# Kernel tuning notes

Measured on AMD Instinct MI355X. Metric: run time of the kernel, lower is better.

The kernel has to match this reference:

```python
import jax, jax.numpy as jnp
import numpy as np

B, N, H = 4, 1024, 32


def setup_inputs() -> dict:
    key = jax.random.key(0)
    ks = jax.random.split(key, 8)
    weights = jax.random.uniform(ks[0], (B, N), dtype=jnp.float32)
    distances = jax.random.uniform(ks[1], (B, N, N), dtype=jnp.float32)
    # nn.Linear-style params (kaiming-uniform-ish scale: U(-1/sqrt(fan_in), 1/sqrt(fan_in)))
    def lin(k, fan_in, fan_out):
        k1, k2 = jax.random.split(k)
        bound = 1.0 / np.sqrt(fan_in)
        W = jax.random.uniform(k1, (fan_in, fan_out), minval=-bound, maxval=bound, dtype=jnp.float32)
        b = jax.random.uniform(k2, (fan_out,), minval=-bound, maxval=bound, dtype=jnp.float32)
        return W, b
    W1, b1 = lin(ks[2], 3, H)
    W2, b2 = lin(ks[3], H, H)
    W3, b3 = lin(ks[4], H, 1)
    return {"weights": weights, "distances": distances,
            "W1": W1, "b1": b1, "W2": W2, "b2": b2, "W3": W3, "b3": b3}


def reference(weights, distances, W1, b1, W2, b2, W3, b3):
    # Avoid materializing the stacked [B,N,N,3] tensor: since the first layer
    # is linear, split W1 rows and broadcast-add the three contributions.
    # h1[b,i,j,:] = w_i * W1[0] + w_j * W1[1] + d_ij * W1[2] + b1
    wi = weights[:, :, None, None] * W1[0]            # [B,N,1,H]
    wj = weights[:, None, :, None] * W1[1]            # [B,1,N,H]
    h = wi + wj + distances[..., None] * W1[2] + b1   # [B,N,N,H]
    h = jax.nn.relu(h)
    h = jax.nn.relu(jnp.einsum('bijh,hk->bijk', h, W2) + b2)
    out = jnp.einsum('bijh,ho->bijo', h, W3) + b3     # [B,N,N,1]
    return jax.nn.softplus(out[..., 0])               # [B,N,N]
```

## Files before the change

kernel.cpp:

```cpp
#include <hip/hip_runtime.h>

#define HCH 32
#define NDIM 1024
#define SEG 512
#define ITERS (SEG / 32)

using half2v  = __attribute__((ext_vector_type(2))) _Float16;
using half8   = __attribute__((ext_vector_type(8))) _Float16;
using floatx4 = __attribute__((ext_vector_type(4))) float;

__global__ __launch_bounds__(256, 4)
void lf_kernel(const float* __restrict__ weights,
               const float* __restrict__ distances,
               const float* __restrict__ W1,
               const float* __restrict__ b1,
               const float* __restrict__ W2,
               const float* __restrict__ b2,
               const float* __restrict__ W3,
               const float* __restrict__ b3,
               float* __restrict__ out)
{
    const int lane = threadIdx.x & 63;
    const int wave_gid = __builtin_amdgcn_readfirstlane(blockIdx.x * 4 + (threadIdx.x >> 6));
    const int row_id = wave_gid >> 1;
    const int j_begin = (wave_gid & 1) * SEG;
    const int b = row_id >> 10;

    const int px = lane & 15;
    const int quad = lane >> 4;
    const int kb = quad * 8;

    const float wi = weights[row_id];

    half2v base2[4], cc2[4], ee2[4];
#pragma unroll
    for (int p = 0; p < 4; ++p) {
        const int chA = kb + 2 * p;
        const int chB = chA + 1;
        base2[p] = half2v{(_Float16)fmaf(W1[chA], wi, b1[chA]),
                          (_Float16)fmaf(W1[chB], wi, b1[chB])};
        cc2[p] = half2v{(_Float16)W1[HCH + chA], (_Float16)W1[HCH + chB]};
        ee2[p] = half2v{(_Float16)W1[2 * HCH + chA], (_Float16)W1[2 * HCH + chB]};
    }

    half8 a_lo, a_hi;
#pragma unroll
    for (int j = 0; j < 8; ++j) {
        a_lo[j] = (_Float16)W2[(kb + j) * HCH + px];
        a_hi[j] = (_Float16)W2[(kb + j) * HCH + 16 + px];
    }

    floatx4 ci_lo, ci_hi;
    float w3lo[4], w3hi[4];
#pragma unroll
    for (int r = 0; r < 4; ++r) {
        ci_lo[r] = b2[quad * 4 + r];
        ci_hi[r] = b2[16 + quad * 4 + r];
        w3lo[r]  = W3[quad * 4 + r];
        w3hi[r]  = W3[16 + quad * 4 + r];
    }
    const float b3v = b3[0];

    const float* __restrict__ drow = distances + (size_t)row_id * NDIM + j_begin;
    const float* __restrict__ wrow = weights + b * NDIM + j_begin;
    float* __restrict__ orow = out + (size_t)row_id * NDIM + j_begin;

    float dbuf[2][2], wbuf[2][2];
#pragma unroll
    for (int t = 0; t < 2; ++t) {
        dbuf[t][0] = drow[t * 32 + px];
        dbuf[t][1] = drow[t * 32 + 16 + px];
        wbuf[t][0] = wrow[t * 32 + px];
        wbuf[t][1] = wrow[t * 32 + 16 + px];
    }

    const half2v zero2 = half2v{(_Float16)0.0f, (_Float16)0.0f};

#pragma unroll
    for (int t = 0; t < ITERS; ++t) {
        const int cur = t & 1;
        const float dA = dbuf[cur][0], dB = dbuf[cur][1];
        const float wA = wbuf[cur][0], wB = wbuf[cur][1];

        const int tp = (t + 2 < ITERS) ? (t + 2) : (t + 2 - ITERS);
        dbuf[cur][0] = drow[tp * 32 + px];
        dbuf[cur][1] = drow[tp * 32 + 16 + px];
        wbuf[cur][0] = wrow[tp * 32 + px];
        wbuf[cur][1] = wrow[tp * 32 + 16 + px];

        const _Float16 dhA = (_Float16)dA, whA = (_Float16)wA;
        const _Float16 dhB = (_Float16)dB, whB = (_Float16)wB;
        const half2v d2A = half2v{dhA, dhA}, w2A = half2v{whA, whA};
        const half2v d2B = half2v{dhB, dhB}, w2B = half2v{whB, whB};

        union Frag { half8 v; half2v h[4]; } fA, fB;
#pragma unroll
        for (int p = 0; p < 4; ++p) {
            half2v tA = __builtin_elementwise_fma(cc2[p], w2A, base2[p]);
            tA = __builtin_elementwise_fma(ee2[p], d2A, tA);
            fA.h[p] = __builtin_elementwise_max(tA, zero2);
            half2v tB = __builtin_elementwise_fma(cc2[p], w2B, base2[p]);
            tB = __builtin_elementwise_fma(ee2[p], d2B, tB);
            fB.h[p] = __builtin_elementwise_max(tB, zero2);
        }

        floatx4 aAlo = __builtin_amdgcn_mfma_f32_16x16x32_f16(a_lo, fA.v, ci_lo, 0, 0, 0);
        floatx4 aAhi = __builtin_amdgcn_mfma_f32_16x16x32_f16(a_hi, fA.v, ci_hi, 0, 0, 0);
        floatx4 aBlo = __builtin_amdgcn_mfma_f32_16x16x32_f16(a_lo, fB.v, ci_lo, 0, 0, 0);
        floatx4 aBhi = __builtin_amdgcn_mfma_f32_16x16x32_f16(a_hi, fB.v, ci_hi, 0, 0, 0);

        float sA = 0.0f, sB = 0.0f;
#pragma unroll
        for (int r = 0; r < 4; ++r) {
            sA = fmaf(fmaxf(aAlo[r], 0.0f), w3lo[r], sA);
            sA = fmaf(fmaxf(aAhi[r], 0.0f), w3hi[r], sA);
            sB = fmaf(fmaxf(aBlo[r], 0.0f), w3lo[r], sB);
            sB = fmaf(fmaxf(aBhi[r], 0.0f), w3hi[r], sB);
        }
        sA += __shfl_xor(sA, 16, 64);
        sA += __shfl_xor(sA, 32, 64);
        sB += __shfl_xor(sB, 16, 64);
        sB += __shfl_xor(sB, 32, 64);

        const float s_sel = (lane & 16) ? sB : sA;
        const float x = s_sel + b3v;
        const float sp = fmaxf(x, 0.0f) + __logf(1.0f + __expf(-fabsf(x)));

        if (lane < 32) orow[t * 32 + lane] = sp;
    }
}

extern "C" void kernel_launch(void* const* d_in, const int* in_sizes, int n_in,
                              void* d_out, int out_size, void* d_ws, size_t ws_size,
                              hipStream_t stream) {
    const float* weights   = (const float*)d_in[0];
    const float* distances = (const float*)d_in[1];
    const float* W1 = (const float*)d_in[2];
    const float* b1 = (const float*)d_in[3];
    const float* W2 = (const float*)d_in[4];
    const float* b2 = (const float*)d_in[5];
    const float* W3 = (const float*)d_in[6];
    const float* b3 = (const float*)d_in[7];
    float* out = (float*)d_out;

    const int rows_total = 4 * 1024;
    dim3 grid(rows_total * (NDIM / SEG) / 4);
    lf_kernel<<<grid, 256, 0, stream>>>(weights, distances, W1, b1, W2, b2, W3, b3, out);
}
```

Baseline: 105.3 us.

## Stage whole row segment into LDS with float4 loads, rotate iteration order

Each wave now loads its whole 512-element distance and weight segment up front with coalesced float4 loads and stores it into per-wave shared memory. The per-iteration scalar global loads and register double-buffering are replaced by LDS reads. The starting iteration is rotated per block, presumably to spread accesses and stores across memory channels, and the occupancy hint goes from 4 to 6. This adds 16 KB of LDS per block, which may cap occupancy, and all loads are now issued up front with no overlap during the loop.

```diff
diff --git a/kernel.cpp b/kernel.cpp
--- a/kernel.cpp
+++ b/kernel.cpp
@@ -9,7 +9,7 @@
 using half8   = __attribute__((ext_vector_type(8))) _Float16;
 using floatx4 = __attribute__((ext_vector_type(4))) float;
 
-__global__ __launch_bounds__(256, 4)
+__global__ __launch_bounds__(256, 6)
 void lf_kernel(const float* __restrict__ weights,
                const float* __restrict__ distances,
                const float* __restrict__ W1,
@@ -20,15 +20,29 @@
                const float* __restrict__ b3,
                float* __restrict__ out)
 {
+    __shared__ float sd[4][SEG];
+    __shared__ float sw[4][SEG];
+
     const int lane = threadIdx.x & 63;
-    const int wave_gid = __builtin_amdgcn_readfirstlane(blockIdx.x * 4 + (threadIdx.x >> 6));
+    const int wv = threadIdx.x >> 6;
+    const int wave_gid = __builtin_amdgcn_readfirstlane(blockIdx.x * 4 + wv);
     const int row_id = wave_gid >> 1;
     const int j_begin = (wave_gid & 1) * SEG;
     const int b = row_id >> 10;
+    const int rot = __builtin_amdgcn_readfirstlane(blockIdx.x & 15);
 
     const int px = lane & 15;
     const int quad = lane >> 4;
     const int kb = quad * 8;
+
+    const float* __restrict__ drow = distances + (size_t)row_id * NDIM + j_begin;
+    const float* __restrict__ wrow = weights + b * NDIM + j_begin;
+    float* __restrict__ orow = out + (size_t)row_id * NDIM + j_begin;
+
+    const float4 dv0 = *(const float4*)(drow + 4 * lane);
+    const float4 dv1 = *(const float4*)(drow + 256 + 4 * lane);
+    const float4 wv0 = *(const float4*)(wrow + 4 * lane);
+    const float4 wv1 = *(const float4*)(wrow + 256 + 4 * lane);
 
     const float wi = weights[row_id];
 
@@ -61,32 +75,22 @@
     }
     const float b3v = b3[0];
 
-    const float* __restrict__ drow = distances + (size_t)row_id * NDIM + j_begin;
-    const float* __restrict__ wrow = weights + b * NDIM + j_begin;
-    float* __restrict__ orow = out + (size_t)row_id * NDIM + j_begin;
-
-    float dbuf[2][2], wbuf[2][2];
-#pragma unroll
-    for (int t = 0; t < 2; ++t) {
-        dbuf[t][0] = drow[t * 32 + px];
-        dbuf[t][1] = drow[t * 32 + 16 + px];
-        wbuf[t][0] = wrow[t * 32 + px];
-        wbuf[t][1] = wrow[t * 32 + 16 + px];
-    }
+    *(float4*)&sd[wv][4 * lane]       = dv0;
+    *(float4*)&sd[wv][256 + 4 * lane] = dv1;
+    *(float4*)&sw[wv][4 * lane]       = wv0;
+    *(float4*)&sw[wv][256 + 4 * lane] = wv1;
 
     const half2v zero2 = half2v{(_Float16)0.0f, (_Float16)0.0f};
 
 #pragma unroll
     for (int t = 0; t < ITERS; ++t) {
-        const int cur = t & 1;
-        const float dA = dbuf[cur][0], dB = dbuf[cur][1];
-        const float wA = wbuf[cur][0], wB = wbuf[cur][1];
+        const int it = (t + rot) & (ITERS - 1);
+        const int base = it * 32;
 
-        const int tp = (t + 2 < ITERS) ? (t + 2) : (t + 2 - ITERS);
-        dbuf[cur][0] = drow[tp * 32 + px];
-        dbuf[cur][1] = drow[tp * 32 + 16 + px];
-        wbuf[cur][0] = wrow[tp * 32 + px];
-        wbuf[cur][1] = wrow[tp * 32 + 16 + px];
+        const float dA = sd[wv][base + px];
+        const float dB = sd[wv][base + 16 + px];
+        const float wA = sw[wv][base + px];
+        const float wB = sw[wv][base + 16 + px];
 
         const _Float16 dhA = (_Float16)dA, whA = (_Float16)wA;
         const _Float16 dhB = (_Float16)dB, whB = (_Float16)wB;
@@ -126,7 +130,7 @@
         const float x = s_sel + b3v;
         const float sp = fmaxf(x, 0.0f) + __logf(1.0f + __expf(-fabsf(x)));
 
-        if (lane < 32) orow[t * 32 + lane] = sp;
+        if (lane < 32) orow[base + lane] = sp;
     }
 }
 
```

Measured after the change: 106.1 us. About the same (+0.8%).
